# Kernel optimization log

Measured on AMD Instinct MI355X. Metric: run time of the kernel, lower is better.

## Reference

```python
import jax, jax.numpy as jnp
import numpy as np

D_MODEL = 1024
NUM_HEADS = 16
HEAD_DIM = D_MODEL // NUM_HEADS


def setup_inputs() -> dict:
    key = jax.random.key(0)
    ks = jax.random.split(key, 11)
    B, S = 2, 2048
    s = 1.0 / np.sqrt(D_MODEL)
    inp = {
        'q': jax.random.normal(ks[0], (B, S, D_MODEL), jnp.float32),
        'k': jax.random.normal(ks[1], (B, S, D_MODEL), jnp.float32),
        'v': jax.random.normal(ks[2], (B, S, D_MODEL), jnp.float32),
        'wq': jax.random.normal(ks[3], (D_MODEL, D_MODEL), jnp.float32) * s,
        'bq': jnp.zeros((D_MODEL,), jnp.float32),
        'wk': jax.random.normal(ks[4], (D_MODEL, D_MODEL), jnp.float32) * s,
        'bk': jnp.zeros((D_MODEL,), jnp.float32),
        'wv': jax.random.normal(ks[5], (D_MODEL, D_MODEL), jnp.float32) * s,
        'bv': jnp.zeros((D_MODEL,), jnp.float32),
        'wo': jax.random.normal(ks[6], (D_MODEL, D_MODEL), jnp.float32) * s,
        'bo': jnp.zeros((D_MODEL,), jnp.float32),
    }
    return inp


def _split_heads(x, B):
    # [B, S, D] -> [B, H, S, Hd]
    return x.reshape(B, -1, NUM_HEADS, HEAD_DIM).transpose(0, 2, 1, 3)


def reference(q, k, v, wq, bq, wk, bk, wv, bv, wo, bo):
    B = q.shape[0]
    qh = _split_heads(q @ wq + bq, B)
    kh = _split_heads(k @ wk + bk, B)
    vh = _split_heads(v @ wv + bv, B)
    scale = 1.0 / np.sqrt(HEAD_DIM).astype(np.float32)
    # [B, H, Sq, Sk]
    scores = jnp.einsum('bhqd,bhkd->bhqk', qh, kh) * scale
    probs = jax.nn.softmax(scores, axis=-1)
    out = jnp.einsum('bhqk,bhkd->bhqd', probs, vh)  # [B, H, Sq, Hd]
    out = out.transpose(0, 2, 1, 3).reshape(B, -1, D_MODEL)
    return out @ wo + bo
```

## Files before the change

### kernel.cpp

```cpp
#include <hip/hip_runtime.h>

typedef unsigned short u16;
typedef __bf16 bf16x8 __attribute__((ext_vector_type(8)));
typedef float    f32x4 __attribute__((ext_vector_type(4)));
typedef float   f32x16 __attribute__((ext_vector_type(16)));
typedef u16      u16x8 __attribute__((ext_vector_type(8)));
typedef u16      u16x4 __attribute__((ext_vector_type(4)));
typedef unsigned uint4v __attribute__((ext_vector_type(4)));

#define DM 1024
#define SQ 2048
#define HD 64
#define QSCALE 0.18033688f

#define SWZ8(row, ch) ((((ch) ^ ((row) & 7) ^ ((row) >> 3)) & 7))
#define SWZ4(row) (((row) >> 1) & 3)

__device__ __forceinline__ u16 f2bf(float f) {
    unsigned u = __builtin_bit_cast(unsigned, f);
    u += 0x7FFFu + ((u >> 16) & 1u);
    return (u16)(u >> 16);
}

__device__ __forceinline__ bf16x8 ldsbf(const u16* p) {
    return __builtin_bit_cast(bf16x8, *(const u16x8*)p);
}

__device__ __forceinline__ unsigned cvtpk(float a, float b) {
    unsigned r;
    asm("v_cvt_pk_bf16_f32 %0, %1, %2" : "=v"(r) : "v"(a), "v"(b));
    return r;
}

__device__ __forceinline__ void swap32(unsigned &a, unsigned &b) {
    asm volatile("v_permlane32_swap_b32 %0, %1" : "+v"(a), "+v"(b));
}

typedef __attribute__((address_space(3))) unsigned lds_u32_t;
typedef __attribute__((address_space(1))) const unsigned glob_u32_t;
__device__ __forceinline__ void gl_lds16(const u16* g, u16* l) {
    __builtin_amdgcn_global_load_lds((glob_u32_t*)g, (lds_u32_t*)l, 16, 0, 0);
}

__global__ __launch_bounds__(256) void convert_kernel(
    const float* __restrict__ q, const float* __restrict__ k,
    const float* __restrict__ v,
    u16* __restrict__ Qc, u16* __restrict__ Kc, u16* __restrict__ Vc)
{
    const int which = blockIdx.x >> 11;
    const float* src = (which==0) ? q : (which==1) ? k : v;
    u16* dst         = (which==0) ? Qc : (which==1) ? Kc : Vc;
    const int off = ((blockIdx.x & 2047) << 11) + threadIdx.x * 8;
    f32x4 x0 = *(const f32x4*)&src[off];
    f32x4 x1 = *(const f32x4*)&src[off + 4];
    u16x8 u;
#pragma unroll
    for (int e = 0; e < 4; ++e) { u[e] = f2bf(x0[e]); u[e+4] = f2bf(x1[e]); }
    *(u16x8*)&dst[off] = u;
}

__global__ __launch_bounds__(256) void wtrans_kernel(
    const float* __restrict__ w0, const float* __restrict__ w1,
    const float* __restrict__ w2, const float* __restrict__ w3,
    u16* __restrict__ t0, u16* __restrict__ t1,
    u16* __restrict__ t2, u16* __restrict__ t3)
{
    __shared__ float tile[32][33];
    const int z = blockIdx.z;
    const float* W = (z==0) ? w0 : (z==1) ? w1 : (z==2) ? w2 : w3;
    u16* T        = (z==0) ? t0 : (z==1) ? t1 : (z==2) ? t2 : t3;
    const float sc = (z==0) ? QSCALE : 1.0f;
    const int tx = threadIdx.x & 31, ty = threadIdx.x >> 5;
    const int n0 = blockIdx.x * 32, k0 = blockIdx.y * 32;
#pragma unroll
    for (int i = 0; i < 4; ++i)
        tile[ty + 8*i][tx] = W[(size_t)(k0 + ty + 8*i)*DM + n0 + tx];
    __syncthreads();
#pragma unroll
    for (int i = 0; i < 4; ++i)
        T[(size_t)(n0 + ty + 8*i)*DM + k0 + tx] = f2bf(tile[tx][ty + 8*i] * sc);
}

template<bool OF32, bool VTLAST>
__global__ __launch_bounds__(256) void gemm_kernel(
    const u16* __restrict__ a0, const u16* __restrict__ a1, const u16* __restrict__ a2,
    const u16* __restrict__ w0, const u16* __restrict__ w1, const u16* __restrict__ w2,
    const float* __restrict__ bi0, const float* __restrict__ bi1, const float* __restrict__ bi2,
    void* __restrict__ o0, void* __restrict__ o1, void* __restrict__ o2,
    float bscale0)
{
    __shared__ __align__(16) u16 As[3][128*32];
    __shared__ __align__(16) u16 Bs[3][128*32];

    const int cpx  = gridDim.x >> 3;
    const int wgid = (blockIdx.x & 7) * cpx + (blockIdx.x >> 3);
    const int z   = wgid >> 8;
    const int rem = wgid & 255;
    const int by  = rem >> 3, bx = rem & 7;

    const u16*  Ap  = (z==0) ? a0 : (z==1) ? a1 : a2;
    const u16*  Wp  = (z==0) ? w0 : (z==1) ? w1 : w2;
    const float* Bp = (z==0) ? bi0 : (z==1) ? bi1 : bi2;
    void* Op        = (z==0) ? o0 : (z==1) ? o1 : o2;
    const float bsc = (z==0) ? bscale0 : 1.0f;

    const int tid  = threadIdx.x;
    const int lane = tid & 63;
    const int wv   = tid >> 6;
    const int m0 = by * 128;
    const int n0 = bx * 128;
    const int wr = (wv >> 1) * 64;
    const int wc = (wv & 1) * 64;
    const int g  = lane >> 4;
    const int mm = lane & 15;

    const int l4r = lane >> 2;
    const int sl  = lane & 3;

    const f32x4 zero4 = {0.f, 0.f, 0.f, 0.f};
    f32x4 acc[4][4];
#pragma unroll
    for (int i = 0; i < 4; ++i)
#pragma unroll
        for (int j = 0; j < 4; ++j) acc[i][j] = zero4;

    auto stageA = [&](int kt, int buf) {
#pragma unroll
        for (int i = 0; i < 2; ++i) {
            const int row = i*64 + wv*16 + l4r;
            const int ch  = sl ^ SWZ4(row);
            gl_lds16(&Ap[(size_t)(m0+row)*DM + kt*32 + ch*8],
                     &As[buf][(i*64 + wv*16)*32]);
        }
    };
    auto stageW = [&](int kt, int buf) {
#pragma unroll
        for (int i = 0; i < 2; ++i) {
            const int row = i*64 + wv*16 + l4r;
            const int ch  = sl ^ SWZ4(row);
            gl_lds16(&Wp[(size_t)(n0+row)*DM + kt*32 + ch*8],
                     &Bs[buf][(i*64 + wv*16)*32]);
        }
    };

    stageA(0, 0); stageW(0, 0);
    stageA(1, 1); stageW(1, 1);

    int cur = 0;
    for (int kt = 0; kt < 32; ++kt) {
        const int nx2 = (cur >= 1) ? cur - 1 : 2;
        if (kt < 30) { stageA(kt + 2, nx2); stageW(kt + 2, nx2); }
        if (kt < 30)      asm volatile("s_waitcnt vmcnt(8)" ::: "memory");
        else if (kt < 31) asm volatile("s_waitcnt vmcnt(4)" ::: "memory");
        else              asm volatile("s_waitcnt vmcnt(0)" ::: "memory");
        __builtin_amdgcn_s_barrier();
        __builtin_amdgcn_sched_barrier(0);

        bf16x8 af[4], bfr[4];
#pragma unroll
        for (int rt = 0; rt < 4; ++rt) {
            const int row = wr + rt*16 + mm;
            af[rt] = ldsbf(&As[cur][row*32 + ((g ^ SWZ4(row)) << 3)]);
        }
#pragma unroll
        for (int ct = 0; ct < 4; ++ct) {
            const int row = wc + ct*16 + mm;
            bfr[ct] = ldsbf(&Bs[cur][row*32 + ((g ^ SWZ4(row)) << 3)]);
        }
        __builtin_amdgcn_s_setprio(1);
#pragma unroll
        for (int rt = 0; rt < 4; ++rt)
#pragma unroll
            for (int ct = 0; ct < 4; ++ct)
                acc[rt][ct] = __builtin_amdgcn_mfma_f32_16x16x32_bf16(
                    af[rt], bfr[ct], acc[rt][ct], 0, 0, 0);
        __builtin_amdgcn_s_setprio(0);

        __builtin_amdgcn_sched_barrier(0);
        __builtin_amdgcn_s_barrier();
        cur = (cur < 2) ? cur + 1 : 0;
    }

    if (VTLAST && z == 2) {
#pragma unroll
        for (int ct = 0; ct < 4; ++ct) {
            const int col = n0 + wc + ct*16 + mm;
            const float bv = Bp[col] * bsc;
#pragma unroll
            for (int rt = 0; rt < 4; ++rt) {
                const int row0 = m0 + wr + rt*16 + g*4;
                const int bb = row0 >> 11, s = row0 & (SQ-1);
                u16x4 pk;
#pragma unroll
                for (int r = 0; r < 4; ++r) pk[r] = f2bf(acc[rt][ct][r] + bv);
                *(u16x4*)&((u16*)Op)[(size_t)(bb*DM + col)*SQ + s] = pk;
            }
        }
    } else {
#pragma unroll
        for (int ct = 0; ct < 4; ++ct) {
            const int col = n0 + wc + ct*16 + mm;
            const float bv = Bp[col] * bsc;
#pragma unroll
            for (int rt = 0; rt < 4; ++rt) {
#pragma unroll
                for (int r = 0; r < 4; ++r) {
                    const int row = m0 + wr + rt*16 + g*4 + r;
                    const float vv = acc[rt][ct][r] + bv;
                    if (OF32) ((float*)Op)[(size_t)row*DM + col] = vv;
                    else      ((u16*) Op)[(size_t)row*DM + col] = f2bf(vv);
                }
            }
        }
    }
}

__global__ __launch_bounds__(512) void attn_kernel(
    const u16* __restrict__ Q, const u16* __restrict__ K,
    const u16* __restrict__ Vt, u16* __restrict__ Z)
{
    __shared__ __align__(16) u16 Kl[2][64*64];
    __shared__ __align__(16) u16 Vl[2][64*64];

    const int tid  = threadIdx.x;
    const int lane = tid & 63;
    const int wid  = tid >> 6;
    const int c    = lane & 31;
    const int hi   = lane >> 5;
    const int srow = tid >> 3;
    const int c8   = tid & 7;

    const int wg = (blockIdx.x & 7) * 32 + (blockIdx.x >> 3);
    const int qt = wg & 7;
    const int hb = wg >> 3;
    const int h  = hb & 15;
    const int b  = hb >> 4;
    const int q0 = qt * 256;

    const size_t kbase = (size_t)(b*SQ)*DM + h*HD;
    const size_t vbase = (size_t)((b*16 + h)*HD)*SQ;

    bf16x8 qf[4];
    {
        const size_t qoff = (size_t)(b*SQ + q0 + wid*32 + c)*DM + h*HD + hi*8;
#pragma unroll
        for (int ks = 0; ks < 4; ++ks)
            qf[ks] = ldsbf(&Q[qoff + ks*16]);
    }

    f32x16 oacc[2];
#pragma unroll
    for (int dt = 0; dt < 2; ++dt)
#pragma unroll
        for (int r = 0; r < 16; ++r) oacc[dt][r] = 0.f;
    f32x16 z16;
#pragma unroll
    for (int r = 0; r < 16; ++r) z16[r] = 0.f;
    float lsp[4] = {0.f, 0.f, 0.f, 0.f};

    const int stw = srow*64 + (SWZ8(srow, c8) << 3);
    u16x8 kreg = *(const u16x8*)&K [kbase + (size_t)srow*DM + c8*8];
    u16x8 vreg = *(const u16x8*)&Vt[vbase + (size_t)srow*SQ + c8*8];
    *(u16x8*)&Kl[0][stw] = kreg;
    *(u16x8*)&Vl[0][stw] = vreg;

    for (int t = 0; t < SQ/64; ++t) {
        const int cur = t & 1;
        __syncthreads();
        if (t + 1 < SQ/64) {
            kreg = *(const u16x8*)&K [kbase + (size_t)((t+1)*64 + srow)*DM + c8*8];
            vreg = *(const u16x8*)&Vt[vbase + (size_t)srow*SQ + (t+1)*64 + c8*8];
        }

        f32x16 pacc[2];
        __builtin_amdgcn_s_setprio(1);
#pragma unroll
        for (int kt = 0; kt < 2; ++kt) {
            const int row = kt*32 + c;
            bf16x8 kf = ldsbf(&Kl[cur][row*64 + (SWZ8(row, hi) << 3)]);
            pacc[kt] = __builtin_amdgcn_mfma_f32_32x32x16_bf16(kf, qf[0], z16, 0, 0, 0);
        }
#pragma unroll
        for (int ks = 1; ks < 4; ++ks) {
#pragma unroll
            for (int kt = 0; kt < 2; ++kt) {
                const int row = kt*32 + c;
                const int ch  = ks*2 + hi;
                bf16x8 kf = ldsbf(&Kl[cur][row*64 + (SWZ8(row, ch) << 3)]);
                pacc[kt] = __builtin_amdgcn_mfma_f32_32x32x16_bf16(kf, qf[ks], pacc[kt], 0, 0, 0);
            }
        }
        __builtin_amdgcn_s_setprio(0);

#pragma unroll
        for (int kt = 0; kt < 2; ++kt)
#pragma unroll
            for (int r = 0; r < 16; ++r) {
                const float e = __builtin_amdgcn_exp2f(pacc[kt][r]);
                pacc[kt][r] = e;
                lsp[r & 3] += e;
            }

        bf16x8 pa[4];
#pragma unroll
        for (int kt = 0; kt < 2; ++kt)
#pragma unroll
            for (int k2 = 0; k2 < 2; ++k2) {
                const int bs = k2*8;
                unsigned u = cvtpk(pacc[kt][bs+0], pacc[kt][bs+1]);
                unsigned v = cvtpk(pacc[kt][bs+2], pacc[kt][bs+3]);
                unsigned w = cvtpk(pacc[kt][bs+4], pacc[kt][bs+5]);
                unsigned x = cvtpk(pacc[kt][bs+6], pacc[kt][bs+7]);
                swap32(u, w);
                swap32(v, x);
                uint4v fr = {u, v, w, x};
                pa[kt*2 + k2] = __builtin_bit_cast(bf16x8, fr);
            }

        __builtin_amdgcn_s_setprio(1);
#pragma unroll
        for (int kp = 0; kp < 4; ++kp) {
#pragma unroll
            for (int dt = 0; dt < 2; ++dt) {
                const int d  = dt*32 + c;
                const int ch = kp*2 + hi;
                bf16x8 vf = ldsbf(&Vl[cur][d*64 + (SWZ8(d, ch) << 3)]);
                oacc[dt] = __builtin_amdgcn_mfma_f32_32x32x16_bf16(pa[kp], vf, oacc[dt], 0, 0, 0);
            }
        }
        __builtin_amdgcn_s_setprio(0);

        if (t + 1 < SQ/64) {
            *(u16x8*)&Kl[cur^1][stw] = kreg;
            *(u16x8*)&Vl[cur^1][stw] = vreg;
        }
    }

    float lsum = (lsp[0] + lsp[1]) + (lsp[2] + lsp[3]);
    lsum += __shfl_xor(lsum, 32, 64);
    const float linv = 1.f / lsum;
    float linvr[16];
#pragma unroll
    for (int r = 0; r < 16; ++r)
        linvr[r] = __shfl(linv, (r & 3) + 8*(r >> 2) + 4*hi, 64);

#pragma unroll
    for (int dt = 0; dt < 2; ++dt)
#pragma unroll
        for (int r = 0; r < 16; ++r) {
            const int qrl = (r & 3) + 8*(r >> 2) + 4*hi;
            const size_t row = (size_t)(b*SQ + q0 + wid*32 + qrl);
            Z[row*DM + h*HD + dt*32 + c] = f2bf(oacc[dt][r] * linvr[r]);
        }
}

extern "C" void kernel_launch(void* const* d_in, const int* in_sizes, int n_in,
                              void* d_out, int out_size, void* d_ws, size_t ws_size,
                              hipStream_t stream)
{
    const float* q  = (const float*)d_in[0];
    const float* k  = (const float*)d_in[1];
    const float* v  = (const float*)d_in[2];
    const float* wq = (const float*)d_in[3];
    const float* bq = (const float*)d_in[4];
    const float* wk = (const float*)d_in[5];
    const float* bk = (const float*)d_in[6];
    const float* wv = (const float*)d_in[7];
    const float* bv = (const float*)d_in[8];
    const float* wo = (const float*)d_in[9];
    const float* bo = (const float*)d_in[10];
    float* out = (float*)d_out;

    char* ws = (char*)d_ws;
    u16* Qc  = (u16*)(ws);
    u16* Kc  = (u16*)(ws + 8388608);
    u16* Vc  = (u16*)(ws + 16777216);
    u16* Qb  = (u16*)(ws + 25165824);
    u16* Kb  = (u16*)(ws + 33554432);
    u16* VtB = (u16*)(ws + 41943040);
    u16* WtQ = (u16*)(ws + 50331648);
    u16* WtK = (u16*)(ws + 52428800);
    u16* WtV = (u16*)(ws + 54525952);
    u16* WtO = (u16*)(ws + 56623104);
    u16* Zb  = Qc;

    wtrans_kernel<<<dim3(32, 32, 4), 256, 0, stream>>>(
        wq, wk, wv, wo, WtQ, WtK, WtV, WtO);

    convert_kernel<<<dim3(3*2048), 256, 0, stream>>>(q, k, v, Qc, Kc, Vc);

    gemm_kernel<false, true><<<dim3(768), 256, 0, stream>>>(
        Qc, Kc, Vc, WtQ, WtK, WtV, bq, bk, bv,
        (void*)Qb, (void*)Kb, (void*)VtB, QSCALE);

    attn_kernel<<<dim3(256), 512, 0, stream>>>(Qb, Kb, VtB, Zb);

    gemm_kernel<true, false><<<dim3(256), 256, 0, stream>>>(
        Zb, Zb, Zb, WtO, WtO, WtO, bo, bo, bo,
        (void*)out, (void*)out, (void*)out, 1.0f);
}
```

Measured before the change: 128.0 us.

## Use 256x256-tile, 8-wave GEMM for fused QKV projection

```diff
diff --git a/kernel.cpp b/kernel.cpp
--- a/kernel.cpp
+++ b/kernel.cpp
@@ -81,28 +81,211 @@
         T[(size_t)(n0 + ty + 8*i)*DM + k0 + tx] = f2bf(tile[tx][ty + 8*i] * sc);
 }
 
-template<bool OF32, bool VTLAST>
-__global__ __launch_bounds__(256) void gemm_kernel(
+template<bool VTLAST>
+__global__ __launch_bounds__(512, 2) void gemm256_kernel(
     const u16* __restrict__ a0, const u16* __restrict__ a1, const u16* __restrict__ a2,
     const u16* __restrict__ w0, const u16* __restrict__ w1, const u16* __restrict__ w2,
     const float* __restrict__ bi0, const float* __restrict__ bi1, const float* __restrict__ bi2,
-    void* __restrict__ o0, void* __restrict__ o1, void* __restrict__ o2,
+    u16* __restrict__ o0, u16* __restrict__ o1, u16* __restrict__ o2,
     float bscale0)
+{
+    __shared__ __align__(16) u16 Al[2][256*64];
+    __shared__ __align__(16) u16 Bl[2][256*64];
+
+    const int wg  = (blockIdx.x & 7) * 24 + (blockIdx.x >> 3);
+    const int z   = wg >> 6;
+    const int rem = wg & 63;
+    const int by  = rem >> 2, bx = rem & 3;
+    const int m0  = by * 256, n0 = bx * 256;
+
+    const u16*  Ap  = (z==0) ? a0 : (z==1) ? a1 : a2;
+    const u16*  Wp  = (z==0) ? w0 : (z==1) ? w1 : w2;
+    const float* Bp = (z==0) ? bi0 : (z==1) ? bi1 : bi2;
+    u16* Op         = (z==0) ? o0 : (z==1) ? o1 : o2;
+    const float bsc = (z==0) ? bscale0 : 1.0f;
+
+    const int tid  = threadIdx.x;
+    const int lane = tid & 63;
+    const int wid  = tid >> 6;
+    const int wr   = (wid >> 2) * 128;
+    const int wc   = (wid & 3) * 64;
+    const int g    = lane >> 4;
+    const int mm   = lane & 15;
+    const int lrow = wid*8 + (lane >> 3);
+    const int tch  = lane & 7;
+
+    f32x4 acc[8][4];
+#pragma unroll
+    for (int i = 0; i < 8; ++i)
+#pragma unroll
+        for (int j = 0; j < 4; ++j) acc[i][j] = f32x4{0.f,0.f,0.f,0.f};
+
+    auto stage = [&](int t, int h) {
+        if (t > 15) return;
+        const int buf  = t & 1;
+        const int rb   = (h & 1) * 128;
+        const u16* sp  = (h < 2) ? Ap : Wp;
+        const int gb   = (h < 2) ? m0 : n0;
+        u16* dp        = ((h < 2) ? &Al[buf][0] : &Bl[buf][0]) + rb*64;
+#pragma unroll
+        for (int i = 0; i < 2; ++i) {
+            const int row = rb + i*64 + lrow;
+            const int ch  = SWZ8(row, tch);
+            gl_lds16(&sp[(size_t)(gb + row)*DM + t*64 + ch*8],
+                     dp + (i*64 + wid*8)*64);
+        }
+    };
+
+    bf16x8 af[4][2], bf0[2][2], bf1[2][2];
+
+    stage(0,0); stage(0,1); stage(0,2); stage(0,3);
+    stage(1,0);
+
+    for (int t = 0; t < 16; ++t) {
+        const int buf = t & 1;
+        const u16* Ab = &Al[buf][0];
+        const u16* Bb = &Bl[buf][0];
+
+        stage(t+1, 1);
+        if (t < 15) asm volatile("s_waitcnt vmcnt(4)" ::: "memory");
+        else        asm volatile("s_waitcnt vmcnt(0)" ::: "memory");
+        __builtin_amdgcn_s_barrier();
+        __builtin_amdgcn_sched_barrier(0);
+#pragma unroll
+        for (int rf = 0; rf < 4; ++rf)
+#pragma unroll
+            for (int kk = 0; kk < 2; ++kk) {
+                const int row = wr + rf*16 + mm;
+                af[rf][kk] = ldsbf(&Ab[row*64 + (SWZ8(row, kk*4+g) << 3)]);
+            }
+#pragma unroll
+        for (int cf = 0; cf < 2; ++cf)
+#pragma unroll
+            for (int kk = 0; kk < 2; ++kk) {
+                const int row = wc + cf*16 + mm;
+                bf0[cf][kk] = ldsbf(&Bb[row*64 + (SWZ8(row, kk*4+g) << 3)]);
+            }
+        __builtin_amdgcn_s_setprio(1);
+#pragma unroll
+        for (int rf = 0; rf < 4; ++rf)
+#pragma unroll
+            for (int cf = 0; cf < 2; ++cf)
+#pragma unroll
+                for (int kk = 0; kk < 2; ++kk)
+                    acc[rf][cf] = __builtin_amdgcn_mfma_f32_16x16x32_bf16(
+                        af[rf][kk], bf0[cf][kk], acc[rf][cf], 0, 0, 0);
+        __builtin_amdgcn_s_setprio(0);
+
+        stage(t+1, 2);
+        __builtin_amdgcn_sched_barrier(0);
+        __builtin_amdgcn_s_barrier();
+        __builtin_amdgcn_sched_barrier(0);
+#pragma unroll
+        for (int cf = 0; cf < 2; ++cf)
+#pragma unroll
+            for (int kk = 0; kk < 2; ++kk) {
+                const int row = wc + 32 + cf*16 + mm;
+                bf1[cf][kk] = ldsbf(&Bb[row*64 + (SWZ8(row, kk*4+g) << 3)]);
+            }
+        __builtin_amdgcn_s_setprio(1);
+#pragma unroll
+        for (int rf = 0; rf < 4; ++rf)
+#pragma unroll
+            for (int cf = 0; cf < 2; ++cf)
+#pragma unroll
+                for (int kk = 0; kk < 2; ++kk)
+                    acc[rf][2+cf] = __builtin_amdgcn_mfma_f32_16x16x32_bf16(
+                        af[rf][kk], bf1[cf][kk], acc[rf][2+cf], 0, 0, 0);
+        __builtin_amdgcn_s_setprio(0);
+
+        stage(t+1, 3);
+        __builtin_amdgcn_sched_barrier(0);
+        __builtin_amdgcn_s_barrier();
+        __builtin_amdgcn_sched_barrier(0);
+#pragma unroll
+        for (int rf = 0; rf < 4; ++rf)
+#pragma unroll
+            for (int kk = 0; kk < 2; ++kk) {
+                const int row = wr + 64 + rf*16 + mm;
+                af[rf][kk] = ldsbf(&Ab[row*64 + (SWZ8(row, kk*4+g) << 3)]);
+            }
+        __builtin_amdgcn_s_setprio(1);
+#pragma unroll
+        for (int rf = 0; rf < 4; ++rf)
+#pragma unroll
+            for (int cf = 0; cf < 2; ++cf)
+#pragma unroll
+                for (int kk = 0; kk < 2; ++kk)
+                    acc[4+rf][2+cf] = __builtin_amdgcn_mfma_f32_16x16x32_bf16(
+                        af[rf][kk], bf1[cf][kk], acc[4+rf][2+cf], 0, 0, 0);
+        __builtin_amdgcn_s_setprio(0);
+
+        stage(t+2, 0);
+        __builtin_amdgcn_sched_barrier(0);
+        __builtin_amdgcn_s_barrier();
+        __builtin_amdgcn_sched_barrier(0);
+        __builtin_amdgcn_s_setprio(1);
+#pragma unroll
+        for (int rf = 0; rf < 4; ++rf)
+#pragma unroll
+            for (int cf = 0; cf < 2; ++cf)
+#pragma unroll
+                for (int kk = 0; kk < 2; ++kk)
+                    acc[4+rf][cf] = __builtin_amdgcn_mfma_f32_16x16x32_bf16(
+                        af[rf][kk], bf0[cf][kk], acc[4+rf][cf], 0, 0, 0);
+        __builtin_amdgcn_s_setprio(0);
+    }
+
+    if (VTLAST && z == 2) {
+#pragma unroll
+        for (int c = 0; c < 4; ++c) {
+            const int col = n0 + wc + c*16 + mm;
+            const float bv = Bp[col] * bsc;
+#pragma unroll
+            for (int f = 0; f < 8; ++f) {
+                const int row0 = m0 + wr + (f>>2)*64 + (f&3)*16 + g*4;
+                const int bb = row0 >> 11, s = row0 & (SQ-1);
+                u16x4 pk;
+#pragma unroll
+                for (int r = 0; r < 4; ++r) pk[r] = f2bf(acc[f][c][r] + bv);
+                *(u16x4*)&Op[(size_t)(bb*DM + col)*SQ + s] = pk;
+            }
+        }
+    } else {
+#pragma unroll
+        for (int c = 0; c < 4; ++c) {
+            const int col = n0 + wc + c*16 + mm;
+            const float bv = Bp[col] * bsc;
+#pragma unroll
+            for (int f = 0; f < 8; ++f) {
+#pragma unroll
+                for (int r = 0; r < 4; ++r) {
+                    const int row = m0 + wr + (f>>2)*64 + (f&3)*16 + g*4 + r;
+                    Op[(size_t)row*DM + col] = f2bf(acc[f][c][r] + bv);
+                }
+            }
+        }
+    }
+}
+
+__global__ __launch_bounds__(256) void gemm128_kernel(
+    const u16* __restrict__ a0,
+    const u16* __restrict__ w0,
+    const float* __restrict__ bi0,
+    float* __restrict__ o0)
 {
     __shared__ __align__(16) u16 As[3][128*32];
     __shared__ __align__(16) u16 Bs[3][128*32];
 
     const int cpx  = gridDim.x >> 3;
     const int wgid = (blockIdx.x & 7) * cpx + (blockIdx.x >> 3);
-    const int z   = wgid >> 8;
     const int rem = wgid & 255;
     const int by  = rem >> 3, bx = rem & 7;
 
-    const u16*  Ap  = (z==0) ? a0 : (z==1) ? a1 : a2;
-    const u16*  Wp  = (z==0) ? w0 : (z==1) ? w1 : w2;
-    const float* Bp = (z==0) ? bi0 : (z==1) ? bi1 : bi2;
-    void* Op        = (z==0) ? o0 : (z==1) ? o1 : o2;
-    const float bsc = (z==0) ? bscale0 : 1.0f;
+    const u16*  Ap  = a0;
+    const u16*  Wp  = w0;
+    const float* Bp = bi0;
+    float* Op       = o0;
 
     const int tid  = threadIdx.x;
     const int lane = tid & 63;
@@ -117,12 +300,11 @@
     const int l4r = lane >> 2;
     const int sl  = lane & 3;
 
-    const f32x4 zero4 = {0.f, 0.f, 0.f, 0.f};
     f32x4 acc[4][4];
 #pragma unroll
     for (int i = 0; i < 4; ++i)
 #pragma unroll
-        for (int j = 0; j < 4; ++j) acc[i][j] = zero4;
+        for (int j = 0; j < 4; ++j) acc[i][j] = f32x4{0.f,0.f,0.f,0.f};
 
     auto stageA = [&](int kt, int buf) {
 #pragma unroll
@@ -181,35 +363,16 @@
         cur = (cur < 2) ? cur + 1 : 0;
     }
 
-    if (VTLAST && z == 2) {
-#pragma unroll
-        for (int ct = 0; ct < 4; ++ct) {
-            const int col = n0 + wc + ct*16 + mm;
-            const float bv = Bp[col] * bsc;
-#pragma unroll
-            for (int rt = 0; rt < 4; ++rt) {
-                const int row0 = m0 + wr + rt*16 + g*4;
-                const int bb = row0 >> 11, s = row0 & (SQ-1);
-                u16x4 pk;
-#pragma unroll
-                for (int r = 0; r < 4; ++r) pk[r] = f2bf(acc[rt][ct][r] + bv);
-                *(u16x4*)&((u16*)Op)[(size_t)(bb*DM + col)*SQ + s] = pk;
-            }
-        }
-    } else {
-#pragma unroll
-        for (int ct = 0; ct < 4; ++ct) {
-            const int col = n0 + wc + ct*16 + mm;
-            const float bv = Bp[col] * bsc;
-#pragma unroll
-            for (int rt = 0; rt < 4; ++rt) {
-#pragma unroll
-                for (int r = 0; r < 4; ++r) {
-                    const int row = m0 + wr + rt*16 + g*4 + r;
-                    const float vv = acc[rt][ct][r] + bv;
-                    if (OF32) ((float*)Op)[(size_t)row*DM + col] = vv;
-                    else      ((u16*) Op)[(size_t)row*DM + col] = f2bf(vv);
-                }
+#pragma unroll
+    for (int ct = 0; ct < 4; ++ct) {
+        const int col = n0 + wc + ct*16 + mm;
+        const float bv = Bp[col];
+#pragma unroll
+        for (int rt = 0; rt < 4; ++rt) {
+#pragma unroll
+            for (int r = 0; r < 4; ++r) {
+                const int row = m0 + wr + rt*16 + g*4 + r;
+                Op[(size_t)row*DM + col] = acc[rt][ct][r] + bv;
             }
         }
     }
@@ -389,13 +552,11 @@
 
     convert_kernel<<<dim3(3*2048), 256, 0, stream>>>(q, k, v, Qc, Kc, Vc);
 
-    gemm_kernel<false, true><<<dim3(768), 256, 0, stream>>>(
+    gemm256_kernel<true><<<dim3(192), 512, 0, stream>>>(
         Qc, Kc, Vc, WtQ, WtK, WtV, bq, bk, bv,
-        (void*)Qb, (void*)Kb, (void*)VtB, QSCALE);
+        Qb, Kb, VtB, QSCALE);
 
     attn_kernel<<<dim3(256), 512, 0, stream>>>(Qb, Kb, VtB, Zb);
 
-    gemm_kernel<true, false><<<dim3(256), 256, 0, stream>>>(
-        Zb, Zb, Zb, WtO, WtO, WtO, bo, bo, bo,
-        (void*)out, (void*)out, (void*)out, 1.0f);
-}
+    gemm128_kernel<<<dim3(256), 256, 0, stream>>>(Zb, WtO, bo, out);
+}
```

Result: no change. 125.5 us (-1.9%).
